# Kernel tuning notes

Measured on AMD Instinct MI355X. Metric: run time of the kernel, lower is better.

The kernel has to match this reference:

```python
import jax, jax.numpy as jnp
import numpy as np
from jax import lax

INPLANES = 512
PLANES = 512
MID = PLANES // 4  # expansion = 4
G = 4              # patch_groups
EPS = 1e-5


def _conv(x, w, groups, pad):
    return lax.conv_general_dilated(
        x, w, window_strides=(1, 1), padding=[(pad, pad), (pad, pad)],
        dimension_numbers=('NCHW', 'OIHW', 'NCHW'), feature_group_count=groups)


def _bn(x, gamma, beta, mean, var):
    scale = gamma / jnp.sqrt(var + EPS)
    return x * scale[None, :, None, None] + (beta - mean * scale)[None, :, None, None]


def _upmask(mask, c, h, w):
    # [b,g,mh,mw] -> repeat each group over c//g channels (group-major channel order),
    # then nearest-upsample to (h, w) (exact integer repeat, matches F.interpolate nearest)
    b, g, mh, mw = mask.shape
    m = jnp.repeat(mask, c // g, axis=1)
    m = jnp.repeat(m, h // mh, axis=2)
    m = jnp.repeat(m, w // mw, axis=3)
    return m


def setup_inputs() -> dict:
    key = jax.random.key(0)
    ks = jax.random.split(key, 20)
    x = jax.random.normal(ks[0], (16, INPLANES, 56, 56), dtype=jnp.float32)
    mask = jax.random.randint(ks[1], (16, G, 7, 7), 0, 2).astype(jnp.float32)
    s = 0.05
    w1 = jax.random.normal(ks[2], (MID, INPLANES // G, 1, 1), dtype=jnp.float32) * s
    w2 = jax.random.normal(ks[3], (MID, MID // G, 3, 3), dtype=jnp.float32) * s
    w3 = jax.random.normal(ks[4], (PLANES, MID // G, 1, 1), dtype=jnp.float32) * s
    def bnp(k, c):
        k1, k2, k3, k4 = jax.random.split(k, 4)
        return (jax.random.normal(k1, (c,), jnp.float32) * 0.1 + 1.0,  # gamma
                jax.random.normal(k2, (c,), jnp.float32) * 0.1,        # beta
                jax.random.normal(k3, (c,), jnp.float32) * 0.1,        # running mean
                jax.random.uniform(k4, (c,), jnp.float32, 0.5, 1.5))   # running var
    g1, b1, m1, v1 = bnp(ks[5], MID)
    g2, b2, m2, v2 = bnp(ks[6], MID)
    g3, b3, m3, v3 = bnp(ks[7], PLANES)
    return dict(x=x, mask=mask, w1=w1, g1=g1, b1=b1, m1=m1, v1=v1,
                w2=w2, g2=g2, b2=b2, m2=m2, v2=v2,
                w3=w3, g3=g3, b3=b3, m3=m3, v3=v3)


def reference(x, mask, w1, g1, b1, m1, v1, w2, g2, b2, m2, v2, w3, g3, b3, m3, v3):
    b, c, h, w = x.shape
    residual = x
    mask1 = _upmask(mask, c, h, w)           # [b, c, h, w]
    out = x * mask1
    out = jax.nn.relu(_bn(_conv(out, w1, G, 0), g1, b1, m1, v1))  # [b, MID, h, w]
    mask2 = _upmask(mask, out.shape[1], h, w)
    out = out * mask2
    out = jax.nn.relu(_bn(_conv(out, w2, G, 1), g2, b2, m2, v2))
    out = out * mask2
    out = _bn(_conv(out, w3, G, 0), g3, b3, m3, v3)
    out = out + residual
    return jax.nn.relu(out)
```

## Files before the change

kernel.cpp:

```cpp
#include <hip/hip_runtime.h>
#include <stdint.h>

typedef unsigned short U16;
typedef unsigned int   U32;
typedef __attribute__((ext_vector_type(8))) short short8;
typedef __attribute__((ext_vector_type(4))) float floatx4;

#define HW 3136

__device__ __forceinline__ U16 f2b(float f){
    union { float f; unsigned int i; } v; v.f = f;
    unsigned int u = (v.i + 0x7FFFu + ((v.i >> 16) & 1u)) >> 16;
    return (U16)u;
}
__device__ __forceinline__ short8 pack8(const float* p){
    float4 a = *reinterpret_cast<const float4*>(p);
    float4 b = *reinterpret_cast<const float4*>(p + 4);
    short8 r;
    r[0]=(short)f2b(a.x); r[1]=(short)f2b(a.y); r[2]=(short)f2b(a.z); r[3]=(short)f2b(a.w);
    r[4]=(short)f2b(b.x); r[5]=(short)f2b(b.y); r[6]=(short)f2b(b.z); r[7]=(short)f2b(b.w);
    return r;
}

__global__ void k_pre(const float* __restrict__ w2,
                      const float* g1, const float* b1, const float* m1, const float* v1,
                      const float* g2, const float* b2, const float* m2, const float* v2,
                      const float* g3, const float* b3, const float* m3, const float* v3,
                      U16* __restrict__ w2t, float* __restrict__ bn){
  int i = blockIdx.x * 256 + threadIdx.x;
  if (i < 4*9*32*32) {
    int ic  = i & 31;
    int oc  = (i >> 5) & 31;
    int gt  = i >> 10;
    int g_  = gt / 9, tap = gt % 9;
    w2t[i] = f2b(w2[((g_*32 + oc)*32 + ic)*9 + tap]);
  } else {
    int j = i - 4*9*32*32;
    if (j >= 768) return;
    const float *gp, *bp, *mp, *vp; int c, so, sho;
    if (j < 128)      { c = j;       gp=g1; bp=b1; mp=m1; vp=v1; so = 0;   sho = 128;  }
    else if (j < 256) { c = j - 128; gp=g2; bp=b2; mp=m2; vp=v2; so = 256; sho = 384;  }
    else              { c = j - 256; gp=g3; bp=b3; mp=m3; vp=v3; so = 512; sho = 1024; }
    float s = gp[c] / sqrtf(vp[c] + 1e-5f);
    bn[so + c]  = s;
    bn[sho + c] = bp[c] - mp[c] * s;
  }
}

__global__ __launch_bounds__(128) void k_conv1(const float* __restrict__ x,
        const float* __restrict__ mask, const float* __restrict__ w1,
        const float* __restrict__ bn, U16* __restrict__ t1){
  const int t = threadIdx.x;
  const int lane = t & 63, wave = t >> 6;
  const int quad = lane >> 4, l15 = lane & 15;
  const int b = blockIdx.z, g = blockIdx.y;
  const int px0 = blockIdx.x*64 + wave*32;
  const float* xg = x + (size_t)(b*512 + g*128)*HW;
  U16* t1g = t1 + (size_t)(b*4 + g)*HW*32;

  int pxl[2]; float mfr[2];
  #pragma unroll
  for (int pxt = 0; pxt < 2; ++pxt){
    int px = px0 + pxt*16 + l15;
    pxl[pxt] = px;
    int h = px / 56, w = px - h*56;
    mfr[pxt] = mask[((b*4 + g)*7 + (h>>3))*7 + (w>>3)];
  }
  const float* wg = w1 + (size_t)(g*32)*128;
  short8 afr[2][4];
  #pragma unroll
  for (int oct = 0; oct < 2; ++oct)
    #pragma unroll
    for (int ks = 0; ks < 4; ++ks)
      afr[oct][ks] = pack8(wg + (oct*16 + l15)*128 + ks*32 + quad*8);

  floatx4 acc[2][2] = {};
  #pragma unroll
  for (int ch = 0; ch < 4; ++ch){
    #pragma unroll
    for (int pxt = 0; pxt < 2; ++pxt){
      const float* bp = xg + (size_t)(ch*32 + quad*8)*HW + pxl[pxt];
      float m = mfr[pxt];
      short8 bfr;
      #pragma unroll
      for (int j = 0; j < 8; ++j)
        bfr[j] = (short)f2b(bp[(size_t)j*HW] * m);
      acc[0][pxt] = __builtin_amdgcn_mfma_f32_16x16x32_bf16(afr[0][ch], bfr, acc[0][pxt], 0,0,0);
      acc[1][pxt] = __builtin_amdgcn_mfma_f32_16x16x32_bf16(afr[1][ch], bfr, acc[1][pxt], 0,0,0);
    }
  }
  #pragma unroll
  for (int oct = 0; oct < 2; ++oct){
    const float* scp = bn + g*32 + oct*16 + quad*4;
    const float* shp = scp + 128;
    #pragma unroll
    for (int pxt = 0; pxt < 2; ++pxt){
      float m = mfr[pxt];
      U16 y[4];
      #pragma unroll
      for (int reg = 0; reg < 4; ++reg)
        y[reg] = f2b(fmaxf(scp[reg]*acc[oct][pxt][reg] + shp[reg], 0.0f) * m);
      uint2 pk = make_uint2((U32)y[0] | ((U32)y[1]<<16), (U32)y[2] | ((U32)y[3]<<16));
      *reinterpret_cast<uint2*>(t1g + (size_t)pxl[pxt]*32 + oct*16 + quad*4) = pk;
    }
  }
}

__global__ __launch_bounds__(256) void k_conv2(const U16* __restrict__ t1,
        const float* __restrict__ mask, const U16* __restrict__ w2t,
        const float* __restrict__ bn, U16* __restrict__ t2){
  const int t = threadIdx.x;
  const int lane = t & 63, wave = t >> 6;
  const int quad = lane >> 4, l15 = lane & 15;
  const int oct = wave & 1;
  const int b = blockIdx.z, g = blockIdx.y;
  const int px0 = blockIdx.x*64 + (wave>>1)*32;
  const U16* tg = t1 + (size_t)(b*4 + g)*HW*32;
  U16*       og = t2 + (size_t)(b*4 + g)*HW*32;

  int pxl[2], hh[2], wwc[2]; float mfr[2];
  #pragma unroll
  for (int pxt = 0; pxt < 2; ++pxt){
    int px = px0 + pxt*16 + l15;
    pxl[pxt] = px;
    int h = px / 56, w = px - h*56;
    hh[pxt] = h; wwc[pxt] = w;
    mfr[pxt] = mask[((b*4 + g)*7 + (h>>3))*7 + (w>>3)];
  }
  const U16* wg = w2t + g*9*32*32;
  floatx4 acc[2] = {};
  #pragma unroll
  for (int kh = 0; kh < 3; ++kh)
    #pragma unroll
    for (int kw = 0; kw < 3; ++kw){
      int tap = kh*3 + kw;
      short8 a = *reinterpret_cast<const short8*>(wg + (tap*32 + oct*16 + l15)*32 + quad*8);
      #pragma unroll
      for (int pxt = 0; pxt < 2; ++pxt){
        int r = hh[pxt] + kh - 1, c = wwc[pxt] + kw - 1;
        short8 bfr;
        #pragma unroll
        for (int j = 0; j < 8; ++j) bfr[j] = 0;
        if ((unsigned)r < 56u && (unsigned)c < 56u)
          bfr = *reinterpret_cast<const short8*>(tg + (size_t)(r*56 + c)*32 + quad*8);
        acc[pxt] = __builtin_amdgcn_mfma_f32_16x16x32_bf16(a, bfr, acc[pxt], 0,0,0);
      }
    }
  const float* scp = bn + 256 + g*32 + oct*16 + quad*4;
  const float* shp = bn + 384 + g*32 + oct*16 + quad*4;
  #pragma unroll
  for (int pxt = 0; pxt < 2; ++pxt){
    float m = mfr[pxt];
    U16 y[4];
    #pragma unroll
    for (int reg = 0; reg < 4; ++reg)
      y[reg] = f2b(fmaxf(scp[reg]*acc[pxt][reg] + shp[reg], 0.0f) * m);
    uint2 pk = make_uint2((U32)y[0] | ((U32)y[1]<<16), (U32)y[2] | ((U32)y[3]<<16));
    *reinterpret_cast<uint2*>(og + (size_t)pxl[pxt]*32 + oct*16 + quad*4) = pk;
  }
}

__global__ __launch_bounds__(256) void k_conv3(const U16* __restrict__ t2,
        const float* __restrict__ x, const float* __restrict__ w3,
        const float* __restrict__ bn, float* __restrict__ out){
  const int t = threadIdx.x;
  const int lane = t & 63, wave = t >> 6;
  const int quad = lane >> 4, l15 = lane & 15;
  const int oh = wave & 1;
  const int b = blockIdx.z, g = blockIdx.y;
  const int px0 = blockIdx.x*64 + (wave>>1)*32;
  const U16* tg = t2 + (size_t)(b*4 + g)*HW*32;
  const float* xg = x + (size_t)(b*512 + g*128)*HW;
  float*       og = out + (size_t)(b*512 + g*128)*HW;

  int pxl[2];
  short8 bfr[2];
  #pragma unroll
  for (int pxt = 0; pxt < 2; ++pxt){
    int px = px0 + pxt*16 + l15;
    pxl[pxt] = px;
    bfr[pxt] = *reinterpret_cast<const short8*>(tg + (size_t)px*32 + quad*8);
  }
  #pragma unroll
  for (int o4 = 0; o4 < 4; ++o4){
    int oct = oh*4 + o4;
    short8 afr = pack8(w3 + (size_t)(g*128 + oct*16 + l15)*32 + quad*8);
    floatx4 acc[2] = {};
    #pragma unroll
    for (int pxt = 0; pxt < 2; ++pxt)
      acc[pxt] = __builtin_amdgcn_mfma_f32_16x16x32_bf16(afr, bfr[pxt], acc[pxt], 0,0,0);
    const float* scp = bn + 512 + g*128 + oct*16 + quad*4;
    const float* shp = bn + 1024 + g*128 + oct*16 + quad*4;
    #pragma unroll
    for (int reg = 0; reg < 4; ++reg){
      int oc = oct*16 + quad*4 + reg;
      float sc = scp[reg], sh = shp[reg];
      #pragma unroll
      for (int pxt = 0; pxt < 2; ++pxt){
        size_t o2 = (size_t)oc*HW + pxl[pxt];
        og[o2] = fmaxf(sc*acc[pxt][reg] + sh + xg[o2], 0.0f);
      }
    }
  }
}

extern "C" void kernel_launch(void* const* d_in, const int* in_sizes, int n_in,
                              void* d_out, int out_size, void* d_ws, size_t ws_size,
                              hipStream_t stream){
  const float* x    = (const float*)d_in[0];
  const float* mask = (const float*)d_in[1];
  const float* w1   = (const float*)d_in[2];
  const float* g1   = (const float*)d_in[3];
  const float* b1   = (const float*)d_in[4];
  const float* m1   = (const float*)d_in[5];
  const float* v1   = (const float*)d_in[6];
  const float* w2   = (const float*)d_in[7];
  const float* g2   = (const float*)d_in[8];
  const float* b2   = (const float*)d_in[9];
  const float* m2   = (const float*)d_in[10];
  const float* v2   = (const float*)d_in[11];
  const float* w3   = (const float*)d_in[12];
  const float* g3   = (const float*)d_in[13];
  const float* b3   = (const float*)d_in[14];
  const float* m3   = (const float*)d_in[15];
  const float* v3   = (const float*)d_in[16];

  char* ws = (char*)d_ws;
  U16*   w2t = (U16*)ws;
  float* bn  = (float*)(ws + 73728);
  U16*   t1  = (U16*)(ws + 79872);
  U16*   t2  = (U16*)(ws + 79872 + 12845056);

  k_pre<<<147, 256, 0, stream>>>(w2, g1,b1,m1,v1, g2,b2,m2,v2, g3,b3,m3,v3, w2t, bn);
  dim3 grid(49, 4, 16);
  k_conv1<<<grid, 128, 0, stream>>>(x, mask, w1, bn, t1);
  k_conv2<<<grid, 256, 0, stream>>>(t1, mask, w2t, bn, t2);
  k_conv3<<<grid, 256, 0, stream>>>(t2, x, w3, bn, (float*)d_out);
}
```

Before: 274.2 us.

## Fuse three grouped conv stages into one kernel with shared-memory tiles and halo

Replaces the three separate conv kernels with a single fused kernel. Each block handles an 8x28 spatial tile per batch and group: conv1 is computed with a halo into LDS, the 3x3 conv2 reads from LDS into a second LDS tile, and conv3 applies the residual and writes the output. This removes the global round trips of the t1 and t2 intermediates and two launches, at the cost of recomputing halo pixels, fewer blocks (896), and higher LDS and register use per block.

New measurement: 408.3 us. 48.9% more time.

```diff
diff --git a/kernel.cpp b/kernel.cpp
--- a/kernel.cpp
+++ b/kernel.cpp
@@ -7,6 +7,7 @@
 typedef __attribute__((ext_vector_type(4))) float floatx4;
 
 #define HW 3136
+#define ICS 40
 
 __device__ __forceinline__ U16 f2b(float f){
     union { float f; unsigned int i; } v; v.f = f;
@@ -47,158 +48,108 @@
   }
 }
 
-__global__ __launch_bounds__(128) void k_conv1(const float* __restrict__ x,
+__global__ __launch_bounds__(512) void k_fused(const float* __restrict__ x,
         const float* __restrict__ mask, const float* __restrict__ w1,
-        const float* __restrict__ bn, U16* __restrict__ t1){
+        const U16* __restrict__ w2t, const float* __restrict__ w3,
+        const float* __restrict__ bn, float* __restrict__ out){
   const int t = threadIdx.x;
-  const int lane = t & 63, wave = t >> 6;
+  const int lane = t & 63, w = t >> 6;
   const int quad = lane >> 4, l15 = lane & 15;
   const int b = blockIdx.z, g = blockIdx.y;
-  const int px0 = blockIdx.x*64 + wave*32;
+  const int mh = blockIdx.x >> 1, half = blockIdx.x & 1;
+  const int h0 = mh*8, c0 = half*28;
+  __shared__ __align__(16) U16 t1s[320*ICS];
+  __shared__ __align__(16) U16 t2s[224*ICS];
   const float* xg = x + (size_t)(b*512 + g*128)*HW;
-  U16* t1g = t1 + (size_t)(b*4 + g)*HW*32;
+  const float* mg = mask + (b*4 + g)*49;
 
-  int pxl[2]; float mfr[2];
-  #pragma unroll
-  for (int pxt = 0; pxt < 2; ++pxt){
-    int px = px0 + pxt*16 + l15;
-    pxl[pxt] = px;
-    int h = px / 56, w = px - h*56;
-    mfr[pxt] = mask[((b*4 + g)*7 + (h>>3))*7 + (w>>3)];
-  }
-  const float* wg = w1 + (size_t)(g*32)*128;
-  short8 afr[2][4];
-  #pragma unroll
-  for (int oct = 0; oct < 2; ++oct)
+  {
+    const int oct = w & 1;
+    const float* wg = w1 + (size_t)(g*32)*128;
+    short8 afr[4];
     #pragma unroll
     for (int ks = 0; ks < 4; ++ks)
-      afr[oct][ks] = pack8(wg + (oct*16 + l15)*128 + ks*32 + quad*8);
-
-  floatx4 acc[2][2] = {};
-  #pragma unroll
-  for (int ch = 0; ch < 4; ++ch){
-    #pragma unroll
-    for (int pxt = 0; pxt < 2; ++pxt){
-      const float* bp = xg + (size_t)(ch*32 + quad*8)*HW + pxl[pxt];
-      float m = mfr[pxt];
-      short8 bfr;
-      #pragma unroll
-      for (int j = 0; j < 8; ++j)
-        bfr[j] = (short)f2b(bp[(size_t)j*HW] * m);
-      acc[0][pxt] = __builtin_amdgcn_mfma_f32_16x16x32_bf16(afr[0][ch], bfr, acc[0][pxt], 0,0,0);
-      acc[1][pxt] = __builtin_amdgcn_mfma_f32_16x16x32_bf16(afr[1][ch], bfr, acc[1][pxt], 0,0,0);
-    }
-  }
-  #pragma unroll
-  for (int oct = 0; oct < 2; ++oct){
+      afr[ks] = pack8(wg + (oct*16 + l15)*128 + ks*32 + quad*8);
     const float* scp = bn + g*32 + oct*16 + quad*4;
     const float* shp = scp + 128;
     #pragma unroll
-    for (int pxt = 0; pxt < 2; ++pxt){
-      float m = mfr[pxt];
+    for (int i = 0; i < 5; ++i){
+      int pt = (w >> 1) + 4*i;
+      int r = pt >> 1, col = (pt & 1)*16 + l15;
+      int hh = h0 - 1 + r, ww = c0 - 2 + col;
+      bool in = ((unsigned)hh < 56u) & ((unsigned)ww < 56u);
+      float m = in ? mg[(hh>>3)*7 + (ww>>3)] : 0.0f;
+      const float* bp = xg + (in ? hh*56 + ww : 0);
+      floatx4 acc = {};
+      #pragma unroll
+      for (int ch = 0; ch < 4; ++ch){
+        short8 bfr;
+        #pragma unroll
+        for (int j = 0; j < 8; ++j)
+          bfr[j] = in ? (short)f2b(bp[(size_t)(ch*32 + quad*8 + j)*HW] * m) : (short)0;
+        acc = __builtin_amdgcn_mfma_f32_16x16x32_bf16(afr[ch], bfr, acc, 0,0,0);
+      }
       U16 y[4];
       #pragma unroll
       for (int reg = 0; reg < 4; ++reg)
-        y[reg] = f2b(fmaxf(scp[reg]*acc[oct][pxt][reg] + shp[reg], 0.0f) * m);
-      uint2 pk = make_uint2((U32)y[0] | ((U32)y[1]<<16), (U32)y[2] | ((U32)y[3]<<16));
-      *reinterpret_cast<uint2*>(t1g + (size_t)pxl[pxt]*32 + oct*16 + quad*4) = pk;
+        y[reg] = f2b(fmaxf(scp[reg]*acc[reg] + shp[reg], 0.0f) * m);
+      *reinterpret_cast<uint2*>(&t1s[(r*32 + col)*ICS + oct*16 + quad*4]) =
+          make_uint2((U32)y[0] | ((U32)y[1]<<16), (U32)y[2] | ((U32)y[3]<<16));
     }
   }
-}
+  __syncthreads();
 
-__global__ __launch_bounds__(256) void k_conv2(const U16* __restrict__ t1,
-        const float* __restrict__ mask, const U16* __restrict__ w2t,
-        const float* __restrict__ bn, U16* __restrict__ t2){
-  const int t = threadIdx.x;
-  const int lane = t & 63, wave = t >> 6;
-  const int quad = lane >> 4, l15 = lane & 15;
-  const int oct = wave & 1;
-  const int b = blockIdx.z, g = blockIdx.y;
-  const int px0 = blockIdx.x*64 + (wave>>1)*32;
-  const U16* tg = t1 + (size_t)(b*4 + g)*HW*32;
-  U16*       og = t2 + (size_t)(b*4 + g)*HW*32;
+  {
+    const int oct = w & 1;
+    const U16* wg2 = w2t + g*9*32*32;
+    const float* scp = bn + 256 + g*32 + oct*16 + quad*4;
+    const float* shp = bn + 384 + g*32 + oct*16 + quad*4;
+    #pragma unroll
+    for (int i = 0; i < 4; ++i){
+      int unit = w + 8*i;
+      if (unit >= 28) break;
+      int px = (unit >> 1)*16 + l15;
+      int r = px / 28, c = px - r*28;
+      float m = mg[((h0 + r)>>3)*7 + ((c0 + c)>>3)];
+      floatx4 acc = {};
+      #pragma unroll
+      for (int kh = 0; kh < 3; ++kh)
+        #pragma unroll
+        for (int kw = 0; kw < 3; ++kw){
+          int tap = kh*3 + kw;
+          short8 a  = *reinterpret_cast<const short8*>(wg2 + (tap*32 + oct*16 + l15)*32 + quad*8);
+          short8 bf = *reinterpret_cast<const short8*>(
+              &t1s[((r + kh)*32 + (c + 1 + kw))*ICS + quad*8]);
+          acc = __builtin_amdgcn_mfma_f32_16x16x32_bf16(a, bf, acc, 0,0,0);
+        }
+      U16 y[4];
+      #pragma unroll
+      for (int reg = 0; reg < 4; ++reg)
+        y[reg] = f2b(fmaxf(scp[reg]*acc[reg] + shp[reg], 0.0f) * m);
+      *reinterpret_cast<uint2*>(&t2s[px*ICS + oct*16 + quad*4]) =
+          make_uint2((U32)y[0] | ((U32)y[1]<<16), (U32)y[2] | ((U32)y[3]<<16));
+    }
+  }
+  __syncthreads();
 
-  int pxl[2], hh[2], wwc[2]; float mfr[2];
-  #pragma unroll
-  for (int pxt = 0; pxt < 2; ++pxt){
-    int px = px0 + pxt*16 + l15;
-    pxl[pxt] = px;
-    int h = px / 56, w = px - h*56;
-    hh[pxt] = h; wwc[pxt] = w;
-    mfr[pxt] = mask[((b*4 + g)*7 + (h>>3))*7 + (w>>3)];
-  }
-  const U16* wg = w2t + g*9*32*32;
-  floatx4 acc[2] = {};
-  #pragma unroll
-  for (int kh = 0; kh < 3; ++kh)
-    #pragma unroll
-    for (int kw = 0; kw < 3; ++kw){
-      int tap = kh*3 + kw;
-      short8 a = *reinterpret_cast<const short8*>(wg + (tap*32 + oct*16 + l15)*32 + quad*8);
-      #pragma unroll
-      for (int pxt = 0; pxt < 2; ++pxt){
-        int r = hh[pxt] + kh - 1, c = wwc[pxt] + kw - 1;
-        short8 bfr;
-        #pragma unroll
-        for (int j = 0; j < 8; ++j) bfr[j] = 0;
-        if ((unsigned)r < 56u && (unsigned)c < 56u)
-          bfr = *reinterpret_cast<const short8*>(tg + (size_t)(r*56 + c)*32 + quad*8);
-        acc[pxt] = __builtin_amdgcn_mfma_f32_16x16x32_bf16(a, bfr, acc[pxt], 0,0,0);
-      }
-    }
-  const float* scp = bn + 256 + g*32 + oct*16 + quad*4;
-  const float* shp = bn + 384 + g*32 + oct*16 + quad*4;
-  #pragma unroll
-  for (int pxt = 0; pxt < 2; ++pxt){
-    float m = mfr[pxt];
-    U16 y[4];
-    #pragma unroll
-    for (int reg = 0; reg < 4; ++reg)
-      y[reg] = f2b(fmaxf(scp[reg]*acc[pxt][reg] + shp[reg], 0.0f) * m);
-    uint2 pk = make_uint2((U32)y[0] | ((U32)y[1]<<16), (U32)y[2] | ((U32)y[3]<<16));
-    *reinterpret_cast<uint2*>(og + (size_t)pxl[pxt]*32 + oct*16 + quad*4) = pk;
-  }
-}
-
-__global__ __launch_bounds__(256) void k_conv3(const U16* __restrict__ t2,
-        const float* __restrict__ x, const float* __restrict__ w3,
-        const float* __restrict__ bn, float* __restrict__ out){
-  const int t = threadIdx.x;
-  const int lane = t & 63, wave = t >> 6;
-  const int quad = lane >> 4, l15 = lane & 15;
-  const int oh = wave & 1;
-  const int b = blockIdx.z, g = blockIdx.y;
-  const int px0 = blockIdx.x*64 + (wave>>1)*32;
-  const U16* tg = t2 + (size_t)(b*4 + g)*HW*32;
-  const float* xg = x + (size_t)(b*512 + g*128)*HW;
-  float*       og = out + (size_t)(b*512 + g*128)*HW;
-
-  int pxl[2];
-  short8 bfr[2];
-  #pragma unroll
-  for (int pxt = 0; pxt < 2; ++pxt){
-    int px = px0 + pxt*16 + l15;
-    pxl[pxt] = px;
-    bfr[pxt] = *reinterpret_cast<const short8*>(tg + (size_t)px*32 + quad*8);
-  }
-  #pragma unroll
-  for (int o4 = 0; o4 < 4; ++o4){
-    int oct = oh*4 + o4;
+  {
+    const int oct = w;
     short8 afr = pack8(w3 + (size_t)(g*128 + oct*16 + l15)*32 + quad*8);
-    floatx4 acc[2] = {};
-    #pragma unroll
-    for (int pxt = 0; pxt < 2; ++pxt)
-      acc[pxt] = __builtin_amdgcn_mfma_f32_16x16x32_bf16(afr, bfr[pxt], acc[pxt], 0,0,0);
     const float* scp = bn + 512 + g*128 + oct*16 + quad*4;
     const float* shp = bn + 1024 + g*128 + oct*16 + quad*4;
+    float* og = out + (size_t)(b*512 + g*128)*HW;
     #pragma unroll
-    for (int reg = 0; reg < 4; ++reg){
-      int oc = oct*16 + quad*4 + reg;
-      float sc = scp[reg], sh = shp[reg];
+    for (int ti = 0; ti < 14; ++ti){
+      int px = ti*16 + l15;
+      int r = px / 28, c = px - r*28;
+      short8 bf = *reinterpret_cast<const short8*>(&t2s[px*ICS + quad*8]);
+      floatx4 acc = {};
+      acc = __builtin_amdgcn_mfma_f32_16x16x32_bf16(afr, bf, acc, 0,0,0);
+      int base = (h0 + r)*56 + c0 + c;
       #pragma unroll
-      for (int pxt = 0; pxt < 2; ++pxt){
-        size_t o2 = (size_t)oc*HW + pxl[pxt];
-        og[o2] = fmaxf(sc*acc[pxt][reg] + sh + xg[o2], 0.0f);
+      for (int reg = 0; reg < 4; ++reg){
+        size_t o2 = (size_t)(oct*16 + quad*4 + reg)*HW + base;
+        og[o2] = fmaxf(scp[reg]*acc[reg] + shp[reg] + xg[o2], 0.0f);
       }
     }
   }
@@ -228,12 +179,8 @@
   char* ws = (char*)d_ws;
   U16*   w2t = (U16*)ws;
   float* bn  = (float*)(ws + 73728);
-  U16*   t1  = (U16*)(ws + 79872);
-  U16*   t2  = (U16*)(ws + 79872 + 12845056);
 
   k_pre<<<147, 256, 0, stream>>>(w2, g1,b1,m1,v1, g2,b2,m2,v2, g3,b3,m3,v3, w2t, bn);
-  dim3 grid(49, 4, 16);
-  k_conv1<<<grid, 128, 0, stream>>>(x, mask, w1, bn, t1);
-  k_conv2<<<grid, 256, 0, stream>>>(t1, mask, w2t, bn, t2);
-  k_conv3<<<grid, 256, 0, stream>>>(t2, x, w3, bn, (float*)d_out);
+  dim3 grid(14, 4, 16);
+  k_fused<<<grid, 512, 0, stream>>>(x, mask, w1, w2t, w3, bn, (float*)d_out);
 }
```
